# Kernel tuning notes

Measured on AMD Instinct MI355X. Metric: run time of the kernel, lower is better.

## Reference

```python
import jax, jax.numpy as jnp
import numpy as np

D_MODEL = 2048
N_HEADS = 16
QK_HEAD_DIM = D_MODEL // N_HEADS  # 128
V_HEAD_DIM = 128
KV_LORA_RANK = 512
EPS = 1e-6
B, S = 2, 2048
ROPE_THETA = 10000.0


def setup_inputs() -> dict:
    key = jax.random.key(0)
    ks = jax.random.split(key, 7)
    x = jax.random.normal(ks[0], (B, S, D_MODEL), dtype=jnp.float32)
    # RoPE frequencies: freqs_cis[s, i] = exp(1j * s * theta^(-2i/d)) -> cos/sin
    inv_freq = 1.0 / (ROPE_THETA ** (np.arange(0, QK_HEAD_DIM, 2, dtype=np.float32) / QK_HEAD_DIM))
    ang = np.arange(S, dtype=np.float32)[:, None] * inv_freq[None, :]  # [S, 64]
    freqs_cos = jnp.asarray(np.cos(ang), dtype=jnp.float32)
    freqs_sin = jnp.asarray(np.sin(ang), dtype=jnp.float32)
    # Parameters stored as [in, out] so that y = x @ W
    def lin(k, fan_in, fan_out):
        return jax.random.normal(k, (fan_in, fan_out), dtype=jnp.float32) / np.sqrt(fan_in)
    w_kv_compress = lin(ks[1], D_MODEL, KV_LORA_RANK)
    kv_norm_w = jnp.ones((KV_LORA_RANK,), dtype=jnp.float32)
    w_k_up = lin(ks[2], KV_LORA_RANK, N_HEADS * QK_HEAD_DIM)
    w_v_up = lin(ks[3], KV_LORA_RANK, N_HEADS * V_HEAD_DIM)
    w_q = lin(ks[4], D_MODEL, N_HEADS * QK_HEAD_DIM)
    w_out = lin(ks[5], N_HEADS * V_HEAD_DIM, D_MODEL)
    return {"x": x, "freqs_cos": freqs_cos, "freqs_sin": freqs_sin,
            "w_kv_compress": w_kv_compress, "kv_norm_w": kv_norm_w,
            "w_k_up": w_k_up, "w_v_up": w_v_up, "w_q": w_q, "w_out": w_out}


def _rms_norm(x, w, eps=EPS):
    var = jnp.mean(jnp.square(x), axis=-1, keepdims=True)
    return x * jax.lax.rsqrt(var + eps) * w


def _apply_rope(t, cos, sin):
    # t: [B, S, H, D]; cos/sin: [S, D//2]; pairs are adjacent elements (complex view)
    b, s, h, d = t.shape
    tr = t.reshape(b, s, h, d // 2, 2)
    x1, x2 = tr[..., 0], tr[..., 1]
    c = cos[None, :, None, :]
    sn = sin[None, :, None, :]
    o1 = x1 * c - x2 * sn
    o2 = x1 * sn + x2 * c
    return jnp.stack([o1, o2], axis=-1).reshape(b, s, h, d)


def reference(x, freqs_cos, freqs_sin, w_kv_compress, kv_norm_w, w_k_up, w_v_up, w_q, w_out):
    b, s, _ = x.shape
    kv_latent = _rms_norm(x @ w_kv_compress, kv_norm_w)      # [B,S,R]
    k = (kv_latent @ w_k_up).reshape(b, s, N_HEADS, QK_HEAD_DIM)
    v = (kv_latent @ w_v_up).reshape(b, s, N_HEADS, V_HEAD_DIM)
    q = (x @ w_q).reshape(b, s, N_HEADS, QK_HEAD_DIM)
    q = _apply_rope(q, freqs_cos, freqs_sin)
    k = _apply_rope(k, freqs_cos, freqs_sin)
    scale = 1.0 / np.sqrt(QK_HEAD_DIM)
    scores = jnp.einsum('bqhd,bkhd->bhqk', q, k) * scale     # [B,H,S,S]
    causal = jnp.tril(jnp.ones((s, s), dtype=bool))
    scores = jnp.where(causal[None, None], scores, jnp.finfo(scores.dtype).min)
    probs = jax.nn.softmax(scores, axis=-1)
    attn = jnp.einsum('bhqk,bkhd->bqhd', probs, v)           # [B,S,H,Dv]
    out = attn.reshape(b, s, N_HEADS * V_HEAD_DIM) @ w_out   # [B,S,d_model]
    return out
```

## Files before the change

### kernel.cpp

```cpp
#include <hip/hip_runtime.h>

typedef unsigned short u16;
typedef __attribute__((ext_vector_type(8))) short bf16x8;
typedef __attribute__((ext_vector_type(4))) float floatx4;

__device__ __forceinline__ float bf2f(u16 h) {
  return __uint_as_float(((unsigned int)h) << 16);
}
__device__ __forceinline__ u16 f2bf(float f) {
  unsigned int u = __float_as_uint(f);
  u += 0x7fffu + ((u >> 16) & 1u);
  return (u16)(u >> 16);
}
__device__ __forceinline__ u16 f2bf_hu(float f) {
  return (u16)((__float_as_uint(f) + 0x8000u) >> 16);
}
__device__ __forceinline__ float exp2fast(float x) {
  float r;
  asm("v_exp_f32 %0, %1" : "=v"(r) : "v"(x));
  return r;
}
__device__ __forceinline__ bool is_f32(const u16* probe) { return probe[0] == 0; }

#define GLOAD_LDS16(gsrc, ldst)                                                        \
  __builtin_amdgcn_global_load_lds(                                                    \
      (const __attribute__((address_space(1))) unsigned int*)(gsrc),                   \
      (__attribute__((address_space(3))) unsigned int*)(ldst), 16, 0, 0)

__global__ __launch_bounds__(256) void cvt_to_bf16(const void* __restrict__ in,
                                                   u16* __restrict__ out, int n,
                                                   const u16* __restrict__ probe) {
  int i = (blockIdx.x * 256 + threadIdx.x) * 8;
  if (i >= n) return;
  if (is_f32(probe)) {
    const float* f = (const float*)in;
    uint4 o;
    o.x = (unsigned)f2bf(f[i + 0]) | ((unsigned)f2bf(f[i + 1]) << 16);
    o.y = (unsigned)f2bf(f[i + 2]) | ((unsigned)f2bf(f[i + 3]) << 16);
    o.z = (unsigned)f2bf(f[i + 4]) | ((unsigned)f2bf(f[i + 5]) << 16);
    o.w = (unsigned)f2bf(f[i + 6]) | ((unsigned)f2bf(f[i + 7]) << 16);
    *(uint4*)(out + i) = o;
  } else {
    *(uint4*)(out + i) = *(const uint4*)((const u16*)in + i);
  }
}

__global__ __launch_bounds__(256) void transpose_cvt(const void* __restrict__ in,
                                                     u16* __restrict__ out,
                                                     int R, int C,
                                                     const u16* __restrict__ probe) {
  __shared__ u16 tile[32][33];
  int bx = blockIdx.x * 32;
  int by = blockIdx.y * 32;
  int tx = threadIdx.x & 31, ty = threadIdx.x >> 5;
  if (is_f32(probe)) {
    const float* f = (const float*)in;
    for (int i = 0; i < 32; i += 8)
      tile[ty + i][tx] = f2bf(f[(size_t)(by + ty + i) * C + (bx + tx)]);
  } else {
    const u16* u = (const u16*)in;
    for (int i = 0; i < 32; i += 8)
      tile[ty + i][tx] = u[(size_t)(by + ty + i) * C + (bx + tx)];
  }
  __syncthreads();
  for (int i = 0; i < 32; i += 8)
    out[(size_t)(bx + ty + i) * R + (by + tx)] = tile[tx][ty + i];
}

__global__ __launch_bounds__(512, 4) void gemm128(const u16* __restrict__ A,
                                                  const u16* __restrict__ BT,
                                                  void* __restrict__ Ca, int sa,
                                                  u16* __restrict__ Cb, int sb,
                                                  int N, int K, int nsplit, int mode,
                                                  const u16* __restrict__ fc,
                                                  const u16* __restrict__ fs,
                                                  float oscale,
                                                  const u16* __restrict__ probe) {
  __shared__ __align__(16) u16 lds[32768];
  u16* const AsB = lds;
  u16* const BsB = lds + 16384;
#define ASLOT(b, k) (AsB + ((((b) << 1) | (k)) << 12))
#define BSLOT(b, k) (BsB + ((((b) << 1) | (k)) << 12))

  const int t = threadIdx.x;
  const int lane = t & 63, wid = t >> 6;
  const int quad = lane >> 4, l16 = lane & 15;
  const int wr = wid >> 2, wc = wid & 3;
  const int m0 = blockIdx.y * 128, n0 = blockIdx.x * 128;
  const int NT = K >> 6;

  const u16* const Abase = A + (size_t)m0 * K;
  const u16* const Bbase = BT + (size_t)n0 * K;

  const int rw = t >> 2;
  const int sg = (t & 3) ^ ((rw & 3) ^ ((rw >> 2) & 3));
  const u16* const sA = Abase + (size_t)rw * K + sg * 8;
  const u16* const sB = Bbase + (size_t)rw * K + sg * 8;
#define STAGE_A(slot, kb) GLOAD_LDS16(sA + (kb), (slot) + t * 8)
#define STAGE_B(slot, kb) GLOAD_LDS16(sB + (kb), (slot) + t * 8)

  const int gofs = (quad ^ ((l16 & 3) ^ ((l16 >> 2) & 3))) * 8;
#define FRAG(slot, row) (*(const bf16x8*)((slot) + (row) * 32 + gofs))

#define SYNC_MID()                                          \
  __builtin_amdgcn_s_barrier();                             \
  asm volatile("s_waitcnt lgkmcnt(0)" ::: "memory");        \
  __builtin_amdgcn_sched_barrier(0)

  floatx4 acc[4][2];
#pragma unroll
  for (int i = 0; i < 4; ++i)
#pragma unroll
    for (int j = 0; j < 2; ++j) acc[i][j] = (floatx4){0.f, 0.f, 0.f, 0.f};

  STAGE_A(ASLOT(0, 0), 0);
  STAGE_B(BSLOT(0, 0), 0);
  STAGE_A(ASLOT(0, 1), 32);
  STAGE_B(BSLOT(0, 1), 32);
  STAGE_A(ASLOT(1, 0), 64);
  STAGE_B(BSLOT(1, 0), 64);
  asm volatile("s_waitcnt vmcnt(2)" ::: "memory");
  __builtin_amdgcn_s_barrier();

  bf16x8 af[4], bfr[2];
  const int arow = wr * 64 + l16;
  const int brow = wc * 32 + l16;

#pragma unroll 1
  for (int u = 0; u < NT; ++u) {
    const int cur = u & 1, oth = cur ^ 1;
    const bool s1 = (u + 1 < NT), s2 = (u + 2 < NT);
    const int kb1 = (u + 1) << 6, kb2 = (u + 2) << 6;

#pragma unroll
    for (int mi = 0; mi < 4; ++mi) af[mi] = FRAG(ASLOT(cur, 0), arow + mi * 16);
#pragma unroll
    for (int nj = 0; nj < 2; ++nj) bfr[nj] = FRAG(BSLOT(cur, 0), brow + nj * 16);
    if (s1) {
      STAGE_A(ASLOT(oth, 1), kb1 + 32);
      STAGE_B(BSLOT(oth, 1), kb1 + 32);
    }
    SYNC_MID();
    __builtin_amdgcn_s_setprio(1);
#pragma unroll
    for (int mi = 0; mi < 4; ++mi)
#pragma unroll
      for (int nj = 0; nj < 2; ++nj)
        acc[mi][nj] = __builtin_amdgcn_mfma_f32_16x16x32_bf16(af[mi], bfr[nj], acc[mi][nj], 0, 0, 0);
    __builtin_amdgcn_s_setprio(0);
    __builtin_amdgcn_sched_barrier(0);
    __builtin_amdgcn_s_barrier();

#pragma unroll
    for (int mi = 0; mi < 4; ++mi) af[mi] = FRAG(ASLOT(cur, 1), arow + mi * 16);
#pragma unroll
    for (int nj = 0; nj < 2; ++nj) bfr[nj] = FRAG(BSLOT(cur, 1), brow + nj * 16);
    if (s2) {
      STAGE_A(ASLOT(cur, 0), kb2);
      STAGE_B(BSLOT(cur, 0), kb2);
    }
    SYNC_MID();
    __builtin_amdgcn_s_setprio(1);
#pragma unroll
    for (int mi = 0; mi < 4; ++mi)
#pragma unroll
      for (int nj = 0; nj < 2; ++nj)
        acc[mi][nj] = __builtin_amdgcn_mfma_f32_16x16x32_bf16(af[mi], bfr[nj], acc[mi][nj], 0, 0, 0);
    __builtin_amdgcn_s_setprio(0);
    __builtin_amdgcn_sched_barrier(0);
    if (s2)
      asm volatile("s_waitcnt vmcnt(2)" ::: "memory");
    else
      asm volatile("s_waitcnt vmcnt(0)" ::: "memory");
    __builtin_amdgcn_s_barrier();
  }

  if (mode == 0) {
    const bool f32o = is_f32(probe);
#pragma unroll
    for (int mi = 0; mi < 4; ++mi) {
      int rbase = m0 + wr * 64 + mi * 16 + quad * 4;
#pragma unroll
      for (int nj = 0; nj < 2; ++nj) {
        int col = n0 + wc * 32 + nj * 16 + l16;
        if (f32o) {
          float* Cf = (float*)Ca;
          for (int r = 0; r < 4; ++r) Cf[(size_t)(rbase + r) * sa + col] = acc[mi][nj][r];
        } else {
          u16* Ch = (u16*)Ca;
          for (int r = 0; r < 4; ++r) Ch[(size_t)(rbase + r) * sa + col] = f2bf(acc[mi][nj][r]);
        }
      }
    }
  } else if (n0 < nsplit) {
    const bool odd = (l16 & 1);
    u16* Ch = (u16*)Ca;
#pragma unroll
    for (int mi = 0; mi < 4; ++mi) {
      int rbase = m0 + wr * 64 + mi * 16 + quad * 4;
#pragma unroll
      for (int nj = 0; nj < 2; ++nj) {
        int col = n0 + wc * 32 + nj * 16 + l16;
        int p = (col & 127) >> 1;
        for (int r = 0; r < 4; ++r) {
          int srow = (rbase + r) & 2047;
          float c = bf2f(fc[srow * 64 + p]);
          float sn = bf2f(fs[srow * 64 + p]);
          float v = acc[mi][nj][r];
          float pv = __shfl_xor(v, 1);
          float o = fmaf(v, c, odd ? pv * sn : -pv * sn);
          Ch[(size_t)(rbase + r) * sa + col] = f2bf(o * oscale);
        }
      }
    }
  } else if (mode == 1) {
#pragma unroll
    for (int mi = 0; mi < 4; ++mi) {
      int rbase = m0 + wr * 64 + mi * 16 + quad * 4;
#pragma unroll
      for (int nj = 0; nj < 2; ++nj) {
        int col = n0 - nsplit + wc * 32 + nj * 16 + l16;
        for (int r = 0; r < 4; ++r)
          Cb[(size_t)(rbase + r) * sb + col] = f2bf(acc[mi][nj][r]);
      }
    }
  } else {
#pragma unroll
    for (int mi = 0; mi < 4; ++mi) {
      int token0 = m0 + wr * 64 + mi * 16 + quad * 4;
#pragma unroll
      for (int nj = 0; nj < 2; ++nj) {
        int ch = n0 - nsplit + wc * 32 + nj * 16 + l16;
        size_t base = (((size_t)((token0 >> 11) * 16 + (ch >> 7)) * 128 + (ch & 127)) << 11) +
                      (token0 & 2047);
        ushort4 pk;
        pk.x = f2bf(acc[mi][nj][0]);
        pk.y = f2bf(acc[mi][nj][1]);
        pk.z = f2bf(acc[mi][nj][2]);
        pk.w = f2bf(acc[mi][nj][3]);
        *(ushort4*)(Cb + base) = pk;
      }
    }
  }
#undef ASLOT
#undef BSLOT
#undef STAGE_A
#undef STAGE_B
#undef FRAG
#undef SYNC_MID
}

__global__ __launch_bounds__(256) void rmsnorm_kernel(u16* __restrict__ t,
                                                      const u16* __restrict__ w) {
  int row = blockIdx.x * 4 + (threadIdx.x >> 6);
  int lane = threadIdx.x & 63;
  u16* xr = t + (size_t)row * 512;
  float v[8];
  float ss = 0.f;
  for (int i = 0; i < 8; ++i) {
    v[i] = bf2f(xr[lane + i * 64]);
    ss += v[i] * v[i];
  }
  for (int d = 32; d > 0; d >>= 1) ss += __shfl_xor(ss, d);
  float r = rsqrtf(ss * (1.f / 512.f) + 1e-6f);
  for (int i = 0; i < 8; ++i) xr[lane + i * 64] = f2bf(v[i] * r * bf2f(w[lane + i * 64]));
}

__global__ __launch_bounds__(256) void attn_kernel(const u16* __restrict__ q,
                                                   const u16* __restrict__ k,
                                                   const u16* __restrict__ vt,
                                                   u16* __restrict__ o) {
  const int S = 2048;
  __shared__ __align__(16) u16 Kt[64 * 128];
  __shared__ __align__(16) u16 Vt[128 * 64];
  __shared__ __align__(16) u16 P[4][16][64];
  const int t = threadIdx.x;
  const int w = t >> 6, lane = t & 63;
  const int quad = lane >> 4, l16 = lane & 15;
  const int bh = blockIdx.x;
  const int b = bh >> 4, h = bh & 15;

  const u16* kbase = k + (size_t)b * S * 2048 + h * 128;
  const u16* vtb = vt + (size_t)bh * 128 * S;

  const int ksrow = t >> 4, ksc = t & 15;
  const int vsrow = t >> 3, vsc = t & 7;

  bf16x8 onesf;
#pragma unroll
  for (int i = 0; i < 8; ++i) onesf[i] = (short)0x3F80;

  const int qb0 = 31 - (int)blockIdx.y;
  const int qb1 = (int)blockIdx.y;

#pragma unroll 1
  for (int qi = 0; qi < 2; ++qi) {
    const int qb = qi ? qb1 : qb0;
    const int q0 = qb * 64 + w * 16;

    const u16* qbase = q + ((size_t)(b * S + q0 + l16)) * 2048 + h * 128;
    bf16x8 qf[4];
    for (int c = 0; c < 4; ++c) qf[c] = *(const bf16x8*)(qbase + c * 32 + quad * 8);

    float m_i[4], l_i[4];
    floatx4 acc[8];
    for (int r = 0; r < 4; ++r) { m_i[r] = -1e30f; l_i[r] = 0.f; }
    for (int nd = 0; nd < 8; ++nd) acc[nd] = (floatx4){0.f, 0.f, 0.f, 0.f};

    const int kmax = q0 + 15;
    const int qbase64 = qb * 64;
    for (int kb = 0; kb <= qbase64; kb += 64) {
      const bool diag = (kb == qbase64);
      __syncthreads();
      for (int j = 0; j < 4; ++j) {
        int row = j * 16 + ksrow;
        GLOAD_LDS16(kbase + (size_t)(kb + row) * 2048 + (ksc ^ (row & 15)) * 8,
                    Kt + (size_t)(row * 16 + ksc) * 8);
      }
      for (int j = 0; j < 4; ++j) {
        int row = j * 32 + vsrow;
        GLOAD_LDS16(vtb + (size_t)row * S + kb + ((vsc ^ (row & 7)) * 8),
                    Vt + (size_t)(row * 8 + vsc) * 8);
      }
      __syncthreads();

      floatx4 s[4];
      if (!diag) {
        for (int ns = 0; ns < 4; ++ns) {
          s[ns] = (floatx4){0.f, 0.f, 0.f, 0.f};
          for (int c = 0; c < 4; ++c) {
            bf16x8 kf = *(const bf16x8*)&Kt[(ns * 16 + l16) * 128 + ((c * 4 + quad) ^ l16) * 8];
            s[ns] = __builtin_amdgcn_mfma_f32_16x16x32_bf16(qf[c], kf, s[ns], 0, 0, 0);
          }
        }
      } else {
        for (int ns = 0; ns < 4; ++ns) {
          if (kb + ns * 16 <= kmax) {
            s[ns] = (floatx4){0.f, 0.f, 0.f, 0.f};
            for (int c = 0; c < 4; ++c) {
              bf16x8 kf = *(const bf16x8*)&Kt[(ns * 16 + l16) * 128 + ((c * 4 + quad) ^ l16) * 8];
              s[ns] = __builtin_amdgcn_mfma_f32_16x16x32_bf16(qf[c], kf, s[ns], 0, 0, 0);
            }
            int key = kb + ns * 16 + l16;
            for (int r = 0; r < 4; ++r)
              s[ns][r] = (key > q0 + quad * 4 + r) ? -1e30f : s[ns][r];
          } else {
            s[ns] = (floatx4){-1e30f, -1e30f, -1e30f, -1e30f};
          }
        }
      }
      float tmax[4];
      for (int r = 0; r < 4; ++r) {
        float v = fmaxf(fmaxf(s[0][r], s[1][r]), fmaxf(s[2][r], s[3][r]));
        for (int d = 1; d < 16; d <<= 1) v = fmaxf(v, __shfl_xor(v, d));
        tmax[r] = v;
      }
      bool grow = (tmax[0] > m_i[0] + 8.f) || (tmax[1] > m_i[1] + 8.f) ||
                  (tmax[2] > m_i[2] + 8.f) || (tmax[3] > m_i[3] + 8.f);
      if (__any(grow)) {
        for (int r = 0; r < 4; ++r) {
          float mn = fmaxf(m_i[r], tmax[r]);
          float alpha = exp2fast(m_i[r] - mn);
          m_i[r] = mn;
          l_i[r] *= alpha;
          for (int nd = 0; nd < 8; ++nd) acc[nd][r] *= alpha;
        }
      }
      for (int ns = 0; ns < 4; ++ns)
        for (int r = 0; r < 4; ++r) s[ns][r] = exp2fast(s[ns][r] - m_i[r]);
      for (int ns = 0; ns < 4; ++ns)
        for (int r = 0; r < 4; ++r) {
          int row = quad * 4 + r;
          P[w][row][(((ns * 2 + (l16 >> 3)) ^ (row & 7)) << 3) | (l16 & 7)] = f2bf_hu(s[ns][r]);
        }
      floatx4 ls = (floatx4){0.f, 0.f, 0.f, 0.f};
      for (int kc = 0; kc < 2; ++kc) {
        if (!diag || kb + kc * 32 <= kmax) {
          bf16x8 pa = *(const bf16x8*)&P[w][l16][((kc * 4 + quad) ^ (l16 & 7)) * 8];
          ls = __builtin_amdgcn_mfma_f32_16x16x32_bf16(pa, onesf, ls, 0, 0, 0);
          for (int nd = 0; nd < 8; ++nd) {
            int d = nd * 16 + l16;
            bf16x8 vf = *(const bf16x8*)&Vt[(d * 8 + ((kc * 4 + quad) ^ (d & 7))) * 8];
            acc[nd] = __builtin_amdgcn_mfma_f32_16x16x32_bf16(pa, vf, acc[nd], 0, 0, 0);
          }
        }
      }
      for (int r = 0; r < 4; ++r) l_i[r] += ls[r];
    }
    u16* ob = o + ((size_t)(b * S + q0 + quad * 4)) * 2048 + h * 128;
    for (int r = 0; r < 4; ++r) {
      float inv = 1.f / l_i[r];
      for (int nd = 0; nd < 8; ++nd)
        ob[(size_t)r * 2048 + nd * 16 + l16] = f2bf(acc[nd][r] * inv);
    }
  }
}

extern "C" void kernel_launch(void* const* d_in, const int* in_sizes, int n_in,
                              void* d_out, int out_size, void* d_ws, size_t ws_size,
                              hipStream_t stream) {
  const void* x    = d_in[0];
  const void* fcos = d_in[1];
  const void* fsin = d_in[2];
  const void* wkv  = d_in[3];
  const void* wnr  = d_in[4];
  const void* wku  = d_in[5];
  const void* wvu  = d_in[6];
  const void* wq   = d_in[7];
  const void* wo   = d_in[8];
  const u16* probe = (const u16*)fcos;

  const size_t MB = 1u << 20;
  char* ws = (char*)d_ws;
  u16* xc    = (u16*)(ws);
  u16* vtb   = (u16*)(ws);
  u16* qb    = (u16*)(ws + 16 * MB);
  u16* kb    = (u16*)(ws + 32 * MB);
  u16* ab    = (u16*)(ws + 48 * MB);
  u16* lat   = (u16*)(ws + 64 * MB);
  u16* wqT   = (u16*)(ws + 68 * MB);
  u16* woT   = (u16*)(ws + 68 * MB);
  u16* wkvT  = (u16*)(ws + 76 * MB);
  u16* wkT   = (u16*)(ws + 78 * MB);
  u16* wvT   = (u16*)(ws + 80 * MB);
  u16* fcosc = (u16*)(ws + 82 * MB);
  u16* fsinc = (u16*)(ws + 82 * MB + 256 * 1024);
  u16* wnrc  = (u16*)(ws + 82 * MB + 512 * 1024);

  const float QSCALE = 0.08838834764831845f * 1.4426950408889634f;
  dim3 blk(256);

  cvt_to_bf16<<<dim3(4096), blk, 0, stream>>>(x, xc, 8388608, probe);
  cvt_to_bf16<<<dim3(64), blk, 0, stream>>>(fcos, fcosc, 131072, probe);
  cvt_to_bf16<<<dim3(64), blk, 0, stream>>>(fsin, fsinc, 131072, probe);
  cvt_to_bf16<<<dim3(1), blk, 0, stream>>>(wnr, wnrc, 512, probe);

  transpose_cvt<<<dim3(64, 64), blk, 0, stream>>>(wq, wqT, 2048, 2048, probe);
  transpose_cvt<<<dim3(16, 64), blk, 0, stream>>>(wkv, wkvT, 2048, 512, probe);

  gemm128<<<dim3(20, 32), dim3(512), 0, stream>>>(xc, wqT, qb, 2048, lat, 512,
                                                  2560, 2048, 2048, 1,
                                                  fcosc, fsinc, QSCALE, probe);
  rmsnorm_kernel<<<dim3(1024), blk, 0, stream>>>(lat, wnrc);

  transpose_cvt<<<dim3(64, 16), blk, 0, stream>>>(wku, wkT, 512, 2048, probe);
  transpose_cvt<<<dim3(64, 16), blk, 0, stream>>>(wvu, wvT, 512, 2048, probe);
  gemm128<<<dim3(32, 32), dim3(512), 0, stream>>>(lat, wkT, kb, 2048, vtb, 0,
                                                  4096, 512, 2048, 2,
                                                  fcosc, fsinc, 1.0f, probe);

  transpose_cvt<<<dim3(64, 64), blk, 0, stream>>>(wo, woT, 2048, 2048, probe);

  attn_kernel<<<dim3(32, 16), blk, 0, stream>>>(qb, kb, vtb, ab);

  gemm128<<<dim3(16, 32), dim3(512), 0, stream>>>(ab, woT, d_out, 2048, nullptr, 0,
                                                  2048, 2048, 0, 0,
                                                  nullptr, nullptr, 1.0f, probe);
}
```

Baseline: 364.2 us.

## Double-buffer K/V tiles in attention kernel with async prefetch

Splits the K and V shared-memory tiles into two buffers. The loads for the next key block are issued before computing on the current one, and a partial vmcnt wait lets compute overlap with global-to-LDS transfers. This adds 32KB of LDS use, which may reduce occupancy. The barrier at the end of each iteration guards buffer reuse. Correctness depends on the vmcnt(8) count matching the number of in-flight loads.

```diff
diff --git a/kernel.cpp b/kernel.cpp
--- a/kernel.cpp
+++ b/kernel.cpp
@@ -271,8 +271,8 @@
                                                    const u16* __restrict__ vt,
                                                    u16* __restrict__ o) {
   const int S = 2048;
-  __shared__ __align__(16) u16 Kt[64 * 128];
-  __shared__ __align__(16) u16 Vt[128 * 64];
+  __shared__ __align__(16) u16 Kt[2][64 * 128];
+  __shared__ __align__(16) u16 Vt[2][128 * 64];
   __shared__ __align__(16) u16 P[4][16][64];
   const int t = threadIdx.x;
   const int w = t >> 6, lane = t & 63;
@@ -308,28 +308,57 @@
     for (int nd = 0; nd < 8; ++nd) acc[nd] = (floatx4){0.f, 0.f, 0.f, 0.f};
 
     const int kmax = q0 + 15;
-    const int qbase64 = qb * 64;
-    for (int kb = 0; kb <= qbase64; kb += 64) {
-      const bool diag = (kb == qbase64);
-      __syncthreads();
-      for (int j = 0; j < 4; ++j) {
-        int row = j * 16 + ksrow;
-        GLOAD_LDS16(kbase + (size_t)(kb + row) * 2048 + (ksc ^ (row & 15)) * 8,
-                    Kt + (size_t)(row * 16 + ksc) * 8);
-      }
-      for (int j = 0; j < 4; ++j) {
-        int row = j * 32 + vsrow;
-        GLOAD_LDS16(vtb + (size_t)row * S + kb + ((vsc ^ (row & 7)) * 8),
-                    Vt + (size_t)(row * 8 + vsc) * 8);
-      }
-      __syncthreads();
+    const int NTI = qb + 1;
+
+#pragma unroll
+    for (int j = 0; j < 4; ++j) {
+      int row = j * 16 + ksrow;
+      GLOAD_LDS16(kbase + (size_t)row * 2048 + (ksc ^ (row & 15)) * 8,
+                  &Kt[0][(size_t)(row * 16 + ksc) * 8]);
+    }
+#pragma unroll
+    for (int j = 0; j < 4; ++j) {
+      int row = j * 32 + vsrow;
+      GLOAD_LDS16(vtb + (size_t)row * S + ((vsc ^ (row & 7)) * 8),
+                  &Vt[0][(size_t)(row * 8 + vsc) * 8]);
+    }
+
+#pragma unroll 1
+    for (int u = 0; u < NTI; ++u) {
+      const int kb = u * 64;
+      const int cur = u & 1, oth = cur ^ 1;
+      const bool diag = (u == NTI - 1);
+      const bool s1 = (u + 1 < NTI);
+
+      if (s1) {
+        const int kb1 = kb + 64;
+#pragma unroll
+        for (int j = 0; j < 4; ++j) {
+          int row = j * 16 + ksrow;
+          GLOAD_LDS16(kbase + (size_t)(kb1 + row) * 2048 + (ksc ^ (row & 15)) * 8,
+                      &Kt[oth][(size_t)(row * 16 + ksc) * 8]);
+        }
+#pragma unroll
+        for (int j = 0; j < 4; ++j) {
+          int row = j * 32 + vsrow;
+          GLOAD_LDS16(vtb + (size_t)row * S + kb1 + ((vsc ^ (row & 7)) * 8),
+                      &Vt[oth][(size_t)(row * 8 + vsc) * 8]);
+        }
+        asm volatile("s_waitcnt vmcnt(8)" ::: "memory");
+      } else {
+        asm volatile("s_waitcnt vmcnt(0)" ::: "memory");
+      }
+      __builtin_amdgcn_s_barrier();
+
+      const u16* Ktc = Kt[cur];
+      const u16* Vtc = Vt[cur];
 
       floatx4 s[4];
       if (!diag) {
         for (int ns = 0; ns < 4; ++ns) {
           s[ns] = (floatx4){0.f, 0.f, 0.f, 0.f};
           for (int c = 0; c < 4; ++c) {
-            bf16x8 kf = *(const bf16x8*)&Kt[(ns * 16 + l16) * 128 + ((c * 4 + quad) ^ l16) * 8];
+            bf16x8 kf = *(const bf16x8*)&Ktc[(ns * 16 + l16) * 128 + ((c * 4 + quad) ^ l16) * 8];
             s[ns] = __builtin_amdgcn_mfma_f32_16x16x32_bf16(qf[c], kf, s[ns], 0, 0, 0);
           }
         }
@@ -338,7 +367,7 @@
           if (kb + ns * 16 <= kmax) {
             s[ns] = (floatx4){0.f, 0.f, 0.f, 0.f};
             for (int c = 0; c < 4; ++c) {
-              bf16x8 kf = *(const bf16x8*)&Kt[(ns * 16 + l16) * 128 + ((c * 4 + quad) ^ l16) * 8];
+              bf16x8 kf = *(const bf16x8*)&Ktc[(ns * 16 + l16) * 128 + ((c * 4 + quad) ^ l16) * 8];
               s[ns] = __builtin_amdgcn_mfma_f32_16x16x32_bf16(qf[c], kf, s[ns], 0, 0, 0);
             }
             int key = kb + ns * 16 + l16;
@@ -380,12 +409,13 @@
           ls = __builtin_amdgcn_mfma_f32_16x16x32_bf16(pa, onesf, ls, 0, 0, 0);
           for (int nd = 0; nd < 8; ++nd) {
             int d = nd * 16 + l16;
-            bf16x8 vf = *(const bf16x8*)&Vt[(d * 8 + ((kc * 4 + quad) ^ (d & 7))) * 8];
+            bf16x8 vf = *(const bf16x8*)&Vtc[(d * 8 + ((kc * 4 + quad) ^ (d & 7))) * 8];
             acc[nd] = __builtin_amdgcn_mfma_f32_16x16x32_bf16(pa, vf, acc[nd], 0, 0, 0);
           }
         }
       }
       for (int r = 0; r < 4; ++r) l_i[r] += ls[r];
+      __builtin_amdgcn_s_barrier();
     }
     u16* ob = o + ((size_t)(b * S + q0 + quad * 4)) * 2048 + h * 128;
     for (int r = 0; r < 4; ++r) {
```

After: 378.2 us. +3.8%, slower.
